# Kernel optimization log

Measured on AMD Instinct MI355X. Metric: run time of the kernel, lower is better.

The kernel has to match this reference:

```python
import jax, jax.numpy as jnp
import numpy as np

D_MODEL = 1024
N_HEADS = 16
HEAD_DIM = D_MODEL // N_HEADS
D_FF = 4096
EPS = 1e-5


def layer_norm(x, w, b):
    mu = jnp.mean(x, axis=-1, keepdims=True)
    var = jnp.var(x, axis=-1, keepdims=True)
    return (x - mu) * jax.lax.rsqrt(var + EPS) * w + b


def setup_inputs() -> dict:
    key = jax.random.key(0)
    ks = jax.random.split(key, 8)
    B, T, C = 2, 2048, D_MODEL
    s = lambda fan_in: 1.0 / np.sqrt(fan_in)
    return {
        "x": jax.random.normal(ks[0], (B, T, C), dtype=jnp.float32),
        "ln1_w": jnp.ones((C,), jnp.float32),
        "ln1_b": jnp.zeros((C,), jnp.float32),
        "qkv_w": jax.random.normal(ks[1], (3 * C, C), jnp.float32) * s(C),
        "attn_out_w": jax.random.normal(ks[2], (C, C), jnp.float32) * s(C),
        "ln2_w": jnp.ones((C,), jnp.float32),
        "ln2_b": jnp.zeros((C,), jnp.float32),
        "mlp_in_w": jax.random.normal(ks[3], (D_FF, C), jnp.float32) * s(C),
        "mlp_gate_w": jax.random.normal(ks[4], (D_FF, C), jnp.float32) * s(C),
        "mlp_out_w": jax.random.normal(ks[5], (C, D_FF), jnp.float32) * s(D_FF),
    }


def reference(x, ln1_w, ln1_b, qkv_w, attn_out_w, ln2_w, ln2_b,
              mlp_in_w, mlp_gate_w, mlp_out_w):
    B, T, C = x.shape
    # --- causal self-attention (pre-norm) ---
    h = layer_norm(x, ln1_w, ln1_b)
    qkv = h @ qkv_w.T  # [B,T,3C]
    q, k, v = jnp.split(qkv, 3, axis=-1)
    def heads(t):
        return t.reshape(B, T, N_HEADS, HEAD_DIM).transpose(0, 2, 1, 3)  # [B,H,T,Dh]
    q, k, v = heads(q), heads(k), heads(v)
    scale = HEAD_DIM ** -0.5
    scores = jnp.einsum("bhqd,bhkd->bhqk", q, k) * scale  # [B,H,T,T]
    causal = jnp.tril(jnp.ones((T, T), dtype=bool))
    scores = jnp.where(causal, scores, -jnp.inf)
    attn = jax.nn.softmax(scores, axis=-1)
    out = jnp.einsum("bhqk,bhkd->bhqd", attn, v)
    out = out.transpose(0, 2, 1, 3).reshape(B, T, C)
    x = x + out @ attn_out_w.T
    # --- SwiGLU MLP (pre-norm) ---
    h = layer_norm(x, ln2_w, ln2_b)
    acts = jax.nn.silu(h @ mlp_in_w.T) * (h @ mlp_gate_w.T)
    return x + acts @ mlp_out_w.T
```

## Files before the change

kernel.cpp:

```cpp
#include <hip/hip_runtime.h>
#include <cstdint>

typedef unsigned short u16;
typedef __bf16 bf16x8 __attribute__((ext_vector_type(8)));
typedef float  f32x4  __attribute__((ext_vector_type(4)));

struct alignas(16) F4 { float v[4]; };
struct alignas(8)  U4 { u16 v[4]; };
struct alignas(16) U8 { u16 v[8]; };

__device__ __forceinline__ u16 f2bf(float f) {
    union { float f; unsigned int u; } x; x.f = f;
    unsigned int r = x.u + 0x7fffu + ((x.u >> 16) & 1u);
    return (u16)(r >> 16);
}
__device__ __forceinline__ float bf2f(u16 u) {
    union { unsigned int u; float f; } x; x.u = ((unsigned int)u) << 16;
    return x.f;
}
__device__ __forceinline__ f32x4 mfma16(bf16x8 a, bf16x8 b, f32x4 c) {
    return __builtin_amdgcn_mfma_f32_16x16x32_bf16(a, b, c, 0, 0, 0);
}
__device__ __forceinline__ bf16x8 ldf(const u16* p) { return *(const bf16x8*)p; }
__device__ __forceinline__ void gload_lds16(const void* g, void* l) {
    auto* gp = reinterpret_cast<const __attribute__((address_space(1))) unsigned int*>(
        reinterpret_cast<uintptr_t>(g));
    auto* lp = reinterpret_cast<__attribute__((address_space(3))) unsigned int*>(
        reinterpret_cast<uintptr_t>(l));
    __builtin_amdgcn_global_load_lds(gp, lp, 16, 0, 0);
}

__global__ __launch_bounds__(256) void cast_bf16_k(const float* __restrict__ in,
                                                   u16* __restrict__ out, int n4) {
    int i = blockIdx.x * 256 + threadIdx.x;
    if (i >= n4) return;
    F4 v = *(const F4*)(in + (size_t)i * 4);
    U4 o;
    #pragma unroll
    for (int j = 0; j < 4; ++j) o.v[j] = f2bf(v.v[j]);
    *(U4*)(out + (size_t)i * 4) = o;
}

__global__ __launch_bounds__(256) void cast_wig_k(const float* __restrict__ wi,
                                                  const float* __restrict__ wg,
                                                  u16* __restrict__ wig) {
    int i = blockIdx.x * 256 + threadIdx.x;
    const int w  = i >> 7;
    const int c8 = (i & 127) * 8;
    const int f  = ((w >> 6) << 5) | (w & 31);
    const float* src = ((w & 32) ? wg : wi) + (size_t)f * 1024 + c8;
    F4 a = *(const F4*)src;
    F4 b = *(const F4*)(src + 4);
    U8 o;
    #pragma unroll
    for (int j = 0; j < 4; ++j) { o.v[j] = f2bf(a.v[j]); o.v[4 + j] = f2bf(b.v[j]); }
    *(U8*)(wig + (size_t)w * 1024 + c8) = o;
}

__global__ __launch_bounds__(256) void ln_fwd_k(const float* __restrict__ x,
                                                const float* __restrict__ w,
                                                const float* __restrict__ b,
                                                u16* __restrict__ h) {
    const int row = blockIdx.x, tid = threadIdx.x;
    const float* xr = x + (size_t)row * 1024;
    F4 v = *(const F4*)(xr + tid * 4);
    float s  = v.v[0] + v.v[1] + v.v[2] + v.v[3];
    float ss = v.v[0]*v.v[0] + v.v[1]*v.v[1] + v.v[2]*v.v[2] + v.v[3]*v.v[3];
    #pragma unroll
    for (int o = 32; o > 0; o >>= 1) { s += __shfl_down(s, o); ss += __shfl_down(ss, o); }
    __shared__ float red[8];
    const int wave = tid >> 6, lane = tid & 63;
    if (lane == 0) { red[wave] = s; red[4 + wave] = ss; }
    __syncthreads();
    s  = red[0] + red[1] + red[2] + red[3];
    ss = red[4] + red[5] + red[6] + red[7];
    const float mu   = s * (1.0f / 1024.0f);
    const float var  = ss * (1.0f / 1024.0f) - mu * mu;
    const float rstd = rsqrtf(var + 1e-5f);
    U4 o;
    #pragma unroll
    for (int j = 0; j < 4; ++j)
        o.v[j] = f2bf((v.v[j] - mu) * rstd * w[tid * 4 + j] + b[tid * 4 + j]);
    *(U4*)(h + (size_t)row * 1024 + tid * 4) = o;
}

template <int MODE>
__global__ __launch_bounds__(256) void gemm_bt_k(const u16* __restrict__ A,
                                                 const u16* __restrict__ Bm,
                                                 void* __restrict__ Cout,
                                                 const float* __restrict__ resid,
                                                 int M, int N, int K) {
    __shared__ u16 Alds[128 * 32];
    __shared__ u16 Blds[128 * 32];
    const int tid  = threadIdx.x;
    const int lane = tid & 63, wave = tid >> 6;
    const int wr = wave >> 1, wc = wave & 1;
    const int r16 = lane & 15, g16 = lane >> 4;
    const int bn = blockIdx.x, bm = blockIdx.y;

    const int srow = lane >> 2;
    const int scol = (lane & 3) * 8;

    f32x4 acc[4][4] = {};

    for (int k0 = 0; k0 < K; k0 += 32) {
        #pragma unroll
        for (int c = 0; c < 2; ++c) {
            const int ch = wave * 2 + c;
            const u16* ga = A  + ((size_t)bm * 128 + ch * 16 + srow) * K + k0 + scol;
            gload_lds16(ga, &Alds[ch * 512]);
            const u16* gb = Bm + ((size_t)bn * 128 + ch * 16 + srow) * K + k0 + scol;
            gload_lds16(gb, &Blds[ch * 512]);
        }
        __syncthreads();
        bf16x8 af[4], bfr[4];
        #pragma unroll
        for (int m = 0; m < 4; ++m)
            af[m] = *(const bf16x8*)&Alds[(wr * 64 + m * 16 + r16) * 32 + g16 * 8];
        #pragma unroll
        for (int n = 0; n < 4; ++n)
            bfr[n] = *(const bf16x8*)&Blds[(wc * 64 + n * 16 + r16) * 32 + g16 * 8];
        #pragma unroll
        for (int m = 0; m < 4; ++m)
            #pragma unroll
            for (int n = 0; n < 4; ++n)
                acc[m][n] = mfma16(af[m], bfr[n], acc[m][n]);
        __syncthreads();
    }

    #pragma unroll
    for (int m = 0; m < 4; ++m) {
        #pragma unroll
        for (int n = 0; n < 4; ++n) {
            #pragma unroll
            for (int r = 0; r < 4; ++r) {
                const int row = bm * 128 + wr * 64 + m * 16 + g16 * 4 + r;
                const int col = bn * 128 + wc * 64 + n * 16 + r16;
                const float v = acc[m][n][r];
                if (MODE == 0) {
                    ((u16*)Cout)[(size_t)row * N + col] = f2bf(v);
                } else {
                    ((float*)Cout)[(size_t)row * N + col] =
                        resid[(size_t)row * N + col] + v;
                }
            }
        }
    }
}

template <int EPI>
__global__ __launch_bounds__(512, 2)
void gemm256_k(const u16* __restrict__ A, const u16* __restrict__ Bm,
               void* __restrict__ Cout, int lda, int ldb, int kLen,
               int nx, int outLd, int planeEls) {
    __shared__ u16 lds[2][2][2][128 * 64];

    const int tid  = threadIdx.x;
    const int wave = tid >> 6, lane = tid & 63;
    const int wm = wave >> 2, wn = wave & 3;
    const int r16 = lane & 15, g16 = lane >> 4;

    const int cpx = gridDim.x >> 3;
    const int swz = (blockIdx.x & 7) * cpx + (blockIdx.x >> 3);
    const int bn = swz % nx, bm = swz / nx;
    const int kBeg = blockIdx.z * kLen;
    const int NT = kLen >> 6;

    const int wr0 = wave * 16 + (lane >> 3);
    const int csw = ((lane & 7) ^ (lane >> 3)) * 8;
    const u16* aP[2][2]; const u16* bP[2][2];
    #pragma unroll
    for (int h = 0; h < 2; ++h) {
        #pragma unroll
        for (int i = 0; i < 2; ++i) {
            const int wr = wr0 + i * 8;
            const int ar = (wr >> 6) * 128 + h * 64 + (wr & 63);
            const int br = (wr >> 5) * 64 + h * 32 + (wr & 31);
            aP[h][i] = A  + (size_t)(bm * 256 + ar) * lda + kBeg + csw;
            bP[h][i] = Bm + (size_t)(bn * 256 + br) * ldb + kBeg + csw;
        }
    }

    auto stA = [&](int kt, int h) {
        u16* d = &lds[kt & 1][0][h][wave * 1024];
        gload_lds16(aP[h][0] + kt * 64, d);
        gload_lds16(aP[h][1] + kt * 64, d + 512);
    };
    auto stB = [&](int kt, int h) {
        u16* d = &lds[kt & 1][1][h][wave * 1024];
        gload_lds16(bP[h][0] + kt * 64, d);
        gload_lds16(bP[h][1] + kt * 64, d + 512);
    };

    int offA[4][2], offB[2][2];
    #pragma unroll
    for (int m = 0; m < 4; ++m)
        #pragma unroll
        for (int ks = 0; ks < 2; ++ks)
            offA[m][ks] = (wm * 64 + m * 16 + r16) * 64 + (((ks * 4 + g16) ^ (r16 & 7)) * 8);
    #pragma unroll
    for (int n = 0; n < 2; ++n)
        #pragma unroll
        for (int ks = 0; ks < 2; ++ks)
            offB[n][ks] = (wn * 32 + n * 16 + r16) * 64 + (((ks * 4 + g16) ^ (r16 & 7)) * 8);

    f32x4 acc[8][4] = {};

    stA(0, 0); stB(0, 0); stB(0, 1); stA(0, 1);
    if (NT > 1) {
        stA(1, 0); stB(1, 0);
        asm volatile("s_waitcnt vmcnt(4)" ::: "memory");
    } else {
        asm volatile("s_waitcnt vmcnt(0)" ::: "memory");
    }
    __builtin_amdgcn_s_barrier();

    for (int kt = 0; kt < NT; ++kt) {
        const int buf = kt & 1;
        const u16* A0 = &lds[buf][0][0][0];
        const u16* A1 = &lds[buf][0][1][0];
        const u16* B0 = &lds[buf][1][0][0];
        const u16* B1 = &lds[buf][1][1][0];
        bf16x8 af[4][2], b0[2][2], b1[2][2];

        #pragma unroll
        for (int m = 0; m < 4; ++m) {
            af[m][0] = ldf(A0 + offA[m][0]);
            af[m][1] = ldf(A0 + offA[m][1]);
        }
        #pragma unroll
        for (int n = 0; n < 2; ++n) {
            b0[n][0] = ldf(B0 + offB[n][0]);
            b0[n][1] = ldf(B0 + offB[n][1]);
        }
        if (kt + 1 < NT) stB(kt + 1, 1);
        __builtin_amdgcn_s_barrier();
        asm volatile("s_waitcnt lgkmcnt(0)" ::: "memory");
        __builtin_amdgcn_s_setprio(1);
        #pragma unroll
        for (int m = 0; m < 4; ++m)
            #pragma unroll
            for (int n = 0; n < 2; ++n) {
                acc[m][n] = mfma16(af[m][0], b0[n][0], acc[m][n]);
                acc[m][n] = mfma16(af[m][1], b0[n][1], acc[m][n]);
            }
        __builtin_amdgcn_s_setprio(0);
        __builtin_amdgcn_s_barrier();

        #pragma unroll
        for (int n = 0; n < 2; ++n) {
            b1[n][0] = ldf(B1 + offB[n][0]);
            b1[n][1] = ldf(B1 + offB[n][1]);
        }
        if (kt + 1 < NT) stA(kt + 1, 1);
        __builtin_amdgcn_s_barrier();
        asm volatile("s_waitcnt lgkmcnt(0)" ::: "memory");
        __builtin_amdgcn_s_setprio(1);
        #pragma unroll
        for (int m = 0; m < 4; ++m)
            #pragma unroll
            for (int n = 0; n < 2; ++n) {
                acc[m][n + 2] = mfma16(af[m][0], b1[n][0], acc[m][n + 2]);
                acc[m][n + 2] = mfma16(af[m][1], b1[n][1], acc[m][n + 2]);
            }
        __builtin_amdgcn_s_setprio(0);
        __builtin_amdgcn_s_barrier();

        #pragma unroll
        for (int m = 0; m < 4; ++m) {
            af[m][0] = ldf(A1 + offA[m][0]);
            af[m][1] = ldf(A1 + offA[m][1]);
        }
        if (kt + 2 < NT) stA(kt + 2, 0);
        __builtin_amdgcn_s_barrier();
        asm volatile("s_waitcnt lgkmcnt(0)" ::: "memory");
        __builtin_amdgcn_s_setprio(1);
        #pragma unroll
        for (int m = 0; m < 4; ++m)
            #pragma unroll
            for (int n = 0; n < 2; ++n) {
                acc[m + 4][n] = mfma16(af[m][0], b0[n][0], acc[m + 4][n]);
                acc[m + 4][n] = mfma16(af[m][1], b0[n][1], acc[m + 4][n]);
            }
        __builtin_amdgcn_s_setprio(0);
        __builtin_amdgcn_s_barrier();

        if (kt + 2 < NT) stB(kt + 2, 0);
        __builtin_amdgcn_s_barrier();
        __builtin_amdgcn_s_setprio(1);
        #pragma unroll
        for (int m = 0; m < 4; ++m)
            #pragma unroll
            for (int n = 0; n < 2; ++n) {
                acc[m + 4][n + 2] = mfma16(af[m][0], b1[n][0], acc[m + 4][n + 2]);
                acc[m + 4][n + 2] = mfma16(af[m][1], b1[n][1], acc[m + 4][n + 2]);
            }
        __builtin_amdgcn_s_setprio(0);
        if (kt + 2 < NT) { asm volatile("s_waitcnt vmcnt(4)" ::: "memory"); }
        else             { asm volatile("s_waitcnt vmcnt(0)" ::: "memory"); }
        __builtin_amdgcn_s_barrier();
    }

    if constexpr (EPI == 1) {
        float* P = (float*)Cout + (size_t)blockIdx.z * planeEls;
        #pragma unroll
        for (int m = 0; m < 8; ++m) {
            #pragma unroll
            for (int n = 0; n < 4; ++n) {
                #pragma unroll
                for (int r = 0; r < 4; ++r) {
                    const int row = bm * 256 + wm * 128 + m * 16 + g16 * 4 + r;
                    const int col = bn * 256 + wn * 64 + n * 16 + r16;
                    P[(size_t)row * outLd + col] = acc[m][n][r];
                }
            }
        }
    } else {
        (void)planeEls;
        u16* O = (u16*)Cout;
        #pragma unroll
        for (int m = 0; m < 8; ++m) {
            #pragma unroll
            for (int n = 0; n < 2; ++n) {
                #pragma unroll
                for (int r = 0; r < 4; ++r) {
                    const int row = bm * 256 + wm * 128 + m * 16 + g16 * 4 + r;
                    const int col = (bn * 4 + wn) * 32 + n * 16 + r16;
                    const float vi = acc[m][n][r];
                    const float vg = acc[m][n + 2][r];
                    const float sl = vi / (1.0f + __expf(-vi));
                    O[(size_t)row * outLd + col] = f2bf(sl * vg);
                }
            }
        }
    }
}

__global__ __launch_bounds__(256) void addreduce4_k(const float* __restrict__ resid,
                                                    const float* __restrict__ p,
                                                    float* __restrict__ out,
                                                    int n4, int planeEls) {
    for (int i = blockIdx.x * 256 + threadIdx.x; i < n4; i += gridDim.x * 256) {
        F4 a = *(const F4*)(resid + (size_t)i * 4);
        F4 b = *(const F4*)(p + (size_t)i * 4);
        F4 c = *(const F4*)(p + (size_t)planeEls + (size_t)i * 4);
        F4 d = *(const F4*)(p + (size_t)2 * planeEls + (size_t)i * 4);
        F4 e = *(const F4*)(p + (size_t)3 * planeEls + (size_t)i * 4);
        F4 o;
        #pragma unroll
        for (int j = 0; j < 4; ++j) o.v[j] = a.v[j] + b.v[j] + c.v[j] + d.v[j] + e.v[j];
        *(F4*)(out + (size_t)i * 4) = o;
    }
}

__global__ __launch_bounds__(256) void attn_fwd_k(const u16* __restrict__ qk,
                                                  const u16* __restrict__ vt,
                                                  u16* __restrict__ Ob) {
    __shared__ u16 Klds[2][64 * 64];
    __shared__ u16 Vlds[2][64 * 64];

    const int tid  = threadIdx.x;
    const int wave = tid >> 6, lane = tid & 63;
    const int r16  = lane & 15, g16 = lane >> 4;

    const int blk = blockIdx.x;
    const int xcd = blk & 7;
    const int pc  = blk >> 3;
    const int hh  = pc >> 5;
    const int qb  = (31 - (pc & 31) + 8 * hh) & 31;
    const int bh  = xcd * 4 + hh;
    const int h   = bh & 15, b = bh >> 4;

    const int q0w = qb * 64 + wave * 16;
    const size_t seqb = (size_t)b * 2048;

    const u16* qp = qk + (seqb + q0w + r16) * 2048 + h * 64 + g16 * 8;
    const bf16x8 qf0 = *(const bf16x8*)qp;
    const bf16x8 qf1 = *(const bf16x8*)(qp + 32);

    const u16* kbase = qk + seqb * 2048 + 1024 + (size_t)h * 64;
    const u16* vbase = vt + (size_t)(h * 64) * 4096 + seqb;

    const int srow  = tid >> 3;
    const int scol8 = ((tid & 7) ^ (srow & 7)) * 8;
    const u16* ksrc = kbase + (size_t)srow * 2048 + scol8;
    const u16* vsrc = vbase + (size_t)srow * 4096 + scol8;

    auto stage = [&](int bufi, int kv0) {
        const u16* kp = ksrc + (size_t)kv0 * 2048;
        const u16* vp = vsrc + kv0;
        u16* kd = &Klds[bufi][wave * 512];
        u16* vd = &Vlds[bufi][wave * 512];
        gload_lds16(kp, kd);
        gload_lds16(kp + (size_t)32 * 2048, kd + 2048);
        gload_lds16(vp, vd);
        gload_lds16(vp + (size_t)32 * 4096, vd + 2048);
    };

    f32x4 o[4] = {};
    float mreg = -3.0e38f, lreg = 0.0f;
    constexpr float SC = 0.125f * 1.44269504088896341f;

    const int nt = qb + 1;
    stage(0, 0);
    asm volatile("s_waitcnt vmcnt(0)" ::: "memory");
    __builtin_amdgcn_s_barrier();

    for (int it = 0; it < nt; ++it) {
        const int kv0 = it * 64;
        const int cur = it & 1;
        if (it + 1 < nt) stage(cur ^ 1, kv0 + 64);

        const u16* K = Klds[cur];
        const u16* V = Vlds[cur];

        f32x4 s[4];
        #pragma unroll
        for (int t = 0; t < 4; ++t) {
            const int row = 16 * t + r16;
            const int sw  = row & 7;
            const bf16x8 k0 = *(const bf16x8*)&K[row * 64 + ((g16 ^ sw) * 8)];
            const bf16x8 k1 = *(const bf16x8*)&K[row * 64 + (((g16 + 4) ^ sw) * 8)];
            f32x4 acc = {0.f, 0.f, 0.f, 0.f};
            acc = mfma16(k0, qf0, acc);
            acc = mfma16(k1, qf1, acc);
            s[t] = acc;
        }

        float a[16];
        #pragma unroll
        for (int t = 0; t < 4; ++t)
            #pragma unroll
            for (int r = 0; r < 4; ++r) a[4 * t + r] = s[t][r] * SC;

        if (kv0 + 63 > q0w) {
            const int qg = q0w + r16;
            #pragma unroll
            for (int t = 0; t < 4; ++t)
                #pragma unroll
                for (int r = 0; r < 4; ++r)
                    if (kv0 + 16 * t + 4 * g16 + r > qg) a[4 * t + r] = -1.0e30f;
        }

        float mx = a[0];
        #pragma unroll
        for (int j = 1; j < 16; ++j) mx = fmaxf(mx, a[j]);
        mx = fmaxf(mx, __shfl_xor(mx, 16));
        mx = fmaxf(mx, __shfl_xor(mx, 32));
        const float mn = fmaxf(mreg, mx);
        const float al = exp2f(mreg - mn);
        float p[16], rs = 0.0f;
        #pragma unroll
        for (int j = 0; j < 16; ++j) { p[j] = exp2f(a[j] - mn); rs += p[j]; }
        rs += __shfl_xor(rs, 16);
        rs += __shfl_xor(rs, 32);
        lreg = lreg * al + rs;
        mreg = mn;

        bf16x8 pf0, pf1;
        #pragma unroll
        for (int j = 0; j < 8; ++j) { pf0[j] = (__bf16)p[j]; pf1[j] = (__bf16)p[8 + j]; }

        #pragma unroll
        for (int t = 0; t < 4; ++t) {
            const int row  = 16 * t + r16;
            const int sw   = row & 7;
            const int base = row * 64 + (g16 & 1) * 4;
            const int c0   = g16 >> 1;
            U4 a0 = *(const U4*)&V[base + (((c0 + 0) ^ sw) * 8)];
            U4 a1 = *(const U4*)&V[base + (((c0 + 2) ^ sw) * 8)];
            U4 b0 = *(const U4*)&V[base + (((c0 + 4) ^ sw) * 8)];
            U4 b1 = *(const U4*)&V[base + (((c0 + 6) ^ sw) * 8)];
            #pragma unroll
            for (int r = 0; r < 4; ++r) o[t][r] *= al;
            bf16x8 v0, v1;
            #pragma unroll
            for (int j = 0; j < 4; ++j) {
                v0[j]     = ((const __bf16*)&a0)[j];
                v0[4 + j] = ((const __bf16*)&a1)[j];
                v1[j]     = ((const __bf16*)&b0)[j];
                v1[4 + j] = ((const __bf16*)&b1)[j];
            }
            o[t] = mfma16(v0, pf0, o[t]);
            o[t] = mfma16(v1, pf1, o[t]);
        }

        if (it + 1 < nt) {
            asm volatile("s_waitcnt vmcnt(0)" ::: "memory");
            __builtin_amdgcn_s_barrier();
        }
    }

    const float inv = 1.0f / lreg;
    u16* op = Ob + (seqb + q0w + r16) * 1024 + h * 64 + 4 * g16;
    #pragma unroll
    for (int t = 0; t < 4; ++t) {
        U4 st;
        #pragma unroll
        for (int r = 0; r < 4; ++r) st.v[r] = f2bf(o[t][r] * inv);
        *(U4*)(op + 16 * t) = st;
    }
}

extern "C" void kernel_launch(void* const* d_in, const int* in_sizes, int n_in,
                              void* d_out, int out_size, void* d_ws, size_t ws_size,
                              hipStream_t stream) {
    (void)in_sizes; (void)n_in; (void)out_size; (void)ws_size;
    constexpr int C = 1024, FF = 4096, M = 2 * 2048;
    constexpr size_t MB = 1024 * 1024;

    const float* x      = (const float*)d_in[0];
    const float* ln1_w  = (const float*)d_in[1];
    const float* ln1_b  = (const float*)d_in[2];
    const float* qkv_w  = (const float*)d_in[3];
    const float* atto_w = (const float*)d_in[4];
    const float* ln2_w  = (const float*)d_in[5];
    const float* ln2_b  = (const float*)d_in[6];
    const float* mlpi_w = (const float*)d_in[7];
    const float* mlpg_w = (const float*)d_in[8];
    const float* mlpo_w = (const float*)d_in[9];
    float* out = (float*)d_out;

    char* ws = (char*)d_ws;
    size_t off = 0;
    auto alloc = [&](size_t bytes) {
        char* p = ws + off;
        off += (bytes + 255) & ~(size_t)255;
        return p;
    };
    u16*   wq   = (u16*)  alloc((size_t)3 * C * C * 2);
    u16*   wo   = (u16*)  alloc((size_t)C * C * 2);
    u16*   wig  = (u16*)  alloc((size_t)2 * FF * C * 2);
    u16*   wm   = (u16*)  alloc((size_t)C * FF * 2);
    float* x1   = (float*)alloc((size_t)M * C * 4);
    u16*   h2   = (u16*)  alloc((size_t)M * C * 2);
    u16*   ab   = (u16*)  alloc((size_t)M * FF * 2);
    char*  R    = alloc(64 * MB);
    u16*   h1   = (u16*)R;
    u16*   qk_b = (u16*)(R + 8 * MB);
    u16*   vt_b = (u16*)(R + 24 * MB);
    u16*   Ob   = (u16*)(R + 32 * MB);
    float* pscr = (float*)R;

    cast_bf16_k<<<(3 * C * C / 4) / 256, 256, 0, stream>>>(qkv_w, wq, 3 * C * C / 4);
    cast_bf16_k<<<(C * C / 4) / 256, 256, 0, stream>>>(atto_w, wo, C * C / 4);
    cast_bf16_k<<<(C * FF / 4) / 256, 256, 0, stream>>>(mlpo_w, wm, C * FF / 4);
    cast_wig_k<<<(2 * FF * C / 8) / 256, 256, 0, stream>>>(mlpi_w, mlpg_w, wig);

    ln_fwd_k<<<M, 256, 0, stream>>>(x, ln1_w, ln1_b, h1);
    gemm_bt_k<0><<<dim3(2 * C / 128, M / 128), 256, 0, stream>>>(h1, wq, qk_b, nullptr, M, 2 * C, C);
    const u16* wv = wq + (size_t)2 * C * C;
    gemm_bt_k<0><<<dim3(M / 128, C / 128), 256, 0, stream>>>(wv, h1, vt_b, nullptr, C, M, C);
    attn_fwd_k<<<1024, 256, 0, stream>>>(qk_b, vt_b, Ob);
    gemm_bt_k<1><<<dim3(C / 128, M / 128), 256, 0, stream>>>(Ob, wo, x1, x, M, C, C);

    ln_fwd_k<<<M, 256, 0, stream>>>(x1, ln2_w, ln2_b, h2);
    gemm256_k<2><<<dim3((2 * FF / 256) * (M / 256), 1, 1), 512, 0, stream>>>(
        h2, wig, ab, C, C, C, 2 * FF / 256, FF, 0);
    gemm256_k<1><<<dim3((C / 256) * (M / 256), 1, 4), 512, 0, stream>>>(
        ab, wm, pscr, FF, FF, FF / 4, C / 256, C, M * C);
    addreduce4_k<<<2048, 256, 0, stream>>>(x1, pscr, out, M * C / 4, M * C);
}
```

Baseline: 304.8 us.

## Prefetch whole tiles two steps ahead and chunk block mapping per XCD

The 256x256 GEMM now stages both k-tiles 0 and 1 up front. Inside the loop it issues the global-to-LDS loads for tile kt+2 in pieces across the four MFMA phases, using fewer barriers and no explicit lgkmcnt waits, to deepen the prefetch and cut synchronisation stalls. The block-index swizzle is also replaced by a mapping that gives each XCD a contiguous rectangle of output tiles, controlled by a new column-chunk parameter, to improve L2 reuse of A and B. The risk is that the reduced barriers open LDS write-after-read hazards, and that more loads in flight raise memory pressure.

```diff
diff --git a/kernel.cpp b/kernel.cpp
--- a/kernel.cpp
+++ b/kernel.cpp
@@ -152,7 +152,7 @@
 __global__ __launch_bounds__(512, 2)
 void gemm256_k(const u16* __restrict__ A, const u16* __restrict__ Bm,
                void* __restrict__ Cout, int lda, int ldb, int kLen,
-               int nx, int outLd, int planeEls) {
+               int nx, int bnCh, int outLd, int planeEls) {
     __shared__ u16 lds[2][2][2][128 * 64];
 
     const int tid  = threadIdx.x;
@@ -161,8 +161,11 @@
     const int r16 = lane & 15, g16 = lane >> 4;
 
     const int cpx = gridDim.x >> 3;
-    const int swz = (blockIdx.x & 7) * cpx + (blockIdx.x >> 3);
-    const int bn = swz % nx, bm = swz / nx;
+    const int xcd = blockIdx.x & 7, loc = blockIdx.x >> 3;
+    const int mCh = cpx / bnCh;
+    const int cpr = nx / bnCh;
+    const int bm = (xcd / cpr) * mCh + loc / bnCh;
+    const int bn = (xcd % cpr) * bnCh + loc % bnCh;
     const int kBeg = blockIdx.z * kLen;
     const int NT = kLen >> 6;
 
@@ -207,12 +210,8 @@
     f32x4 acc[8][4] = {};
 
     stA(0, 0); stB(0, 0); stB(0, 1); stA(0, 1);
-    if (NT > 1) {
-        stA(1, 0); stB(1, 0);
-        asm volatile("s_waitcnt vmcnt(4)" ::: "memory");
-    } else {
-        asm volatile("s_waitcnt vmcnt(0)" ::: "memory");
-    }
+    stA(1, 0); stB(1, 0); stB(1, 1); stA(1, 1);
+    asm volatile("s_waitcnt vmcnt(8)" ::: "memory");
     __builtin_amdgcn_s_barrier();
 
     for (int kt = 0; kt < NT; ++kt) {
@@ -221,6 +220,7 @@
         const u16* A1 = &lds[buf][0][1][0];
         const u16* B0 = &lds[buf][1][0][0];
         const u16* B1 = &lds[buf][1][1][0];
+        const bool pf = (kt + 2 < NT);
         bf16x8 af[4][2], b0[2][2], b1[2][2];
 
         #pragma unroll
@@ -233,9 +233,6 @@
             b0[n][0] = ldf(B0 + offB[n][0]);
             b0[n][1] = ldf(B0 + offB[n][1]);
         }
-        if (kt + 1 < NT) stB(kt + 1, 1);
-        __builtin_amdgcn_s_barrier();
-        asm volatile("s_waitcnt lgkmcnt(0)" ::: "memory");
         __builtin_amdgcn_s_setprio(1);
         #pragma unroll
         for (int m = 0; m < 4; ++m)
@@ -252,9 +249,7 @@
             b1[n][0] = ldf(B1 + offB[n][0]);
             b1[n][1] = ldf(B1 + offB[n][1]);
         }
-        if (kt + 1 < NT) stA(kt + 1, 1);
-        __builtin_amdgcn_s_barrier();
-        asm volatile("s_waitcnt lgkmcnt(0)" ::: "memory");
+        if (pf) { stA(kt + 2, 0); stB(kt + 2, 0); }
         __builtin_amdgcn_s_setprio(1);
         #pragma unroll
         for (int m = 0; m < 4; ++m)
@@ -271,9 +266,7 @@
             af[m][0] = ldf(A1 + offA[m][0]);
             af[m][1] = ldf(A1 + offA[m][1]);
         }
-        if (kt + 2 < NT) stA(kt + 2, 0);
-        __builtin_amdgcn_s_barrier();
-        asm volatile("s_waitcnt lgkmcnt(0)" ::: "memory");
+        if (pf) stB(kt + 2, 1);
         __builtin_amdgcn_s_setprio(1);
         #pragma unroll
         for (int m = 0; m < 4; ++m)
@@ -285,8 +278,7 @@
         __builtin_amdgcn_s_setprio(0);
         __builtin_amdgcn_s_barrier();
 
-        if (kt + 2 < NT) stB(kt + 2, 0);
-        __builtin_amdgcn_s_barrier();
+        if (pf) stA(kt + 2, 1);
         __builtin_amdgcn_s_setprio(1);
         #pragma unroll
         for (int m = 0; m < 4; ++m)
@@ -296,9 +288,9 @@
                 acc[m + 4][n + 2] = mfma16(af[m][1], b1[n][1], acc[m + 4][n + 2]);
             }
         __builtin_amdgcn_s_setprio(0);
-        if (kt + 2 < NT) { asm volatile("s_waitcnt vmcnt(4)" ::: "memory"); }
-        else             { asm volatile("s_waitcnt vmcnt(0)" ::: "memory"); }
-        __builtin_amdgcn_s_barrier();
+        if (pf)                   { asm volatile("s_waitcnt vmcnt(8)" ::: "memory"); }
+        else if (kt + 1 < NT)     { asm volatile("s_waitcnt vmcnt(0)" ::: "memory"); }
+        if (kt + 1 < NT) __builtin_amdgcn_s_barrier();
     }
 
     if constexpr (EPI == 1) {
@@ -556,8 +548,8 @@
 
     ln_fwd_k<<<M, 256, 0, stream>>>(x1, ln2_w, ln2_b, h2);
     gemm256_k<2><<<dim3((2 * FF / 256) * (M / 256), 1, 1), 512, 0, stream>>>(
-        h2, wig, ab, C, C, C, 2 * FF / 256, FF, 0);
+        h2, wig, ab, C, C, C, 2 * FF / 256, 8, FF, 0);
     gemm256_k<1><<<dim3((C / 256) * (M / 256), 1, 4), 512, 0, stream>>>(
-        ab, wm, pscr, FF, FF, FF / 4, C / 256, C, M * C);
+        ab, wm, pscr, FF, FF, FF / 4, C / 256, 4, C, M * C);
     addreduce4_k<<<2048, 256, 0, stream>>>(x1, pscr, out, M * C / 4, M * C);
 }
```

Result: faster. 297.4 us (-2.4%).
